# Kernel optimization log

Hardware: AMD Instinct MI355X
Metric: run time of the kernel (lower is better)

Reference implementation:

```python
import jax, jax.numpy as jnp
import numpy as np

# Standard NF4 lookup table (16 quantile values of a normal distribution)
NF4_TABLE = jnp.array([
    -1.0, -0.6961928009986877, -0.5250730514526367, -0.39491748809814453,
    -0.28444138169288635, -0.18477343022823334, -0.09105003625154495, 0.0,
    0.07958029955625534, 0.16093020141124725, 0.24611230194568634,
    0.33791524171829224, 0.44070982933044434, 0.5626170039176941,
    0.7229568362236023, 1.0], dtype=jnp.float32)
BLOCK = 64  # per-block quantization block size


def dequant_nf4(codes, scalers):
    """codes: int [out, in] values in [0,16); scalers: float [out*in/BLOCK]."""
    shape = codes.shape
    vals = NF4_TABLE[codes.reshape(-1, BLOCK)]  # [n_blocks, BLOCK]
    return (vals * scalers[:, None]).reshape(shape)


def setup_inputs() -> dict:
    key = jax.random.key(0)
    ks = jax.random.split(key, 7)
    D, H, T = 4096, 11008, 8192
    nb1 = H * D // BLOCK
    x = jax.random.normal(ks[0], (T, D), dtype=jnp.float32)
    w1_codes = jax.random.randint(ks[1], (H, D), 0, 16, dtype=jnp.int32)
    w1_scalers = jax.random.uniform(ks[2], (nb1,), dtype=jnp.float32) * 0.02
    w2_codes = jax.random.randint(ks[3], (H, D), 0, 16, dtype=jnp.int32)
    w2_scalers = jax.random.uniform(ks[4], (nb1,), dtype=jnp.float32) * 0.02
    w3_codes = jax.random.randint(ks[5], (D, H), 0, 16, dtype=jnp.int32)
    w3_scalers = jax.random.uniform(ks[6], (nb1,), dtype=jnp.float32) * 0.02
    return {"x": x, "w1_codes": w1_codes, "w1_scalers": w1_scalers,
            "w2_codes": w2_codes, "w2_scalers": w2_scalers,
            "w3_codes": w3_codes, "w3_scalers": w3_scalers}


def reference(x, w1_codes, w1_scalers, w2_codes, w2_scalers, w3_codes, w3_scalers):
    w1 = dequant_nf4(w1_codes, w1_scalers)  # [H, D]
    w2 = dequant_nf4(w2_codes, w2_scalers)  # [H, D]
    w3 = dequant_nf4(w3_codes, w3_scalers)  # [D, H]
    h = jax.nn.silu(x @ w1.T) * (x @ w2.T)  # [T, H]
    return h @ w3.T                          # [T, D]
```

## Files before the change

### kernel.cpp

```cpp
#include <hip/hip_runtime.h>
#include <hip/hip_bf16.h>

#define T_DIM 8192
#define D_DIM 4096
#define H_DIM 11008

typedef __attribute__((ext_vector_type(8))) __bf16 bf16x8;
typedef __attribute__((ext_vector_type(4))) float f32x4;

typedef __attribute__((address_space(1))) const void gvoid_t;
typedef __attribute__((address_space(3))) void lvoid_t;

__device__ __forceinline__ void async_lds16(const void* g, void* l) {
    __builtin_amdgcn_global_load_lds((gvoid_t*)g, (lvoid_t*)l, 16, 0, 0);
}

__device__ const float NF4_TAB[16] = {
    -1.0f, -0.6961928009986877f, -0.5250730514526367f, -0.39491748809814453f,
    -0.28444138169288635f, -0.18477343022823334f, -0.09105003625154495f, 0.0f,
    0.07958029955625534f, 0.16093020141124725f, 0.24611230194568634f,
    0.33791524171829224f, 0.44070982933044434f, 0.5626170039176941f,
    0.7229568362236023f, 1.0f};

__global__ void dequant_nf4_kernel(const int* __restrict__ codes,
                                   const float* __restrict__ scalers,
                                   __bf16* __restrict__ out, long n) {
    __shared__ float tbl[16];
    if (threadIdx.x < 16) tbl[threadIdx.x] = NF4_TAB[threadIdx.x];
    __syncthreads();
    long i = ((long)blockIdx.x * blockDim.x + threadIdx.x) * 8;
    if (i >= n) return;
    float s = scalers[i >> 6];
    const int4* cp = (const int4*)(codes + i);
    int4 c0 = cp[0], c1 = cp[1];
    bf16x8 v;
    v[0] = (__bf16)(tbl[c0.x] * s);
    v[1] = (__bf16)(tbl[c0.y] * s);
    v[2] = (__bf16)(tbl[c0.z] * s);
    v[3] = (__bf16)(tbl[c0.w] * s);
    v[4] = (__bf16)(tbl[c1.x] * s);
    v[5] = (__bf16)(tbl[c1.y] * s);
    v[6] = (__bf16)(tbl[c1.z] * s);
    v[7] = (__bf16)(tbl[c1.w] * s);
    *(bf16x8*)(out + i) = v;
}

__global__ void cvt_f32_bf16(const float* __restrict__ x, __bf16* __restrict__ out, long n) {
    long i = ((long)blockIdx.x * blockDim.x + threadIdx.x) * 8;
    if (i >= n) return;
    const float4* xp = (const float4*)(x + i);
    float4 f0 = xp[0], f1 = xp[1];
    bf16x8 v;
    v[0] = (__bf16)f0.x; v[1] = (__bf16)f0.y; v[2] = (__bf16)f0.z; v[3] = (__bf16)f0.w;
    v[4] = (__bf16)f1.x; v[5] = (__bf16)f1.y; v[6] = (__bf16)f1.z; v[7] = (__bf16)f1.w;
    *(bf16x8*)(out + i) = v;
}

template<int KD, int SILU, typename OutT>
__global__ __launch_bounds__(512, 2) void gemm_nt(
    const __bf16* __restrict__ A, const __bf16* __restrict__ B1,
    const __bf16* __restrict__ B2, OutT* __restrict__ Out, const int N)
{
    static_assert(KD % 128 == 0, "need an even number of K-tiles");
    __shared__ __bf16 lds[2 * 2 * 256 * 64];

    const int tid  = threadIdx.x;
    const int lane = tid & 63;
    const int wave = tid >> 6;
    const int wm = wave >> 2;
    const int wn = wave & 3;

    const int nwg  = gridDim.x * gridDim.y;
    const int bid0 = blockIdx.y * gridDim.x + blockIdx.x;
    const int q    = nwg >> 3;
    const int Rr   = q / gridDim.x;
    const int xcd  = bid0 & 7;
    const int j    = bid0 >> 3;
    const int by   = xcd * Rr + (j % Rr);
    const int bx   = j / Rr;
    const long m0 = (long)by * 256;
    const long n0 = (long)bx * (SILU ? 128 : 256);

    const int sr = tid >> 3;
    const int sb = (tid & 7) ^ (sr & 7);
    const __bf16* Arow = A + (m0 + sr) * (long)KD + sb * 8;
    const __bf16* Brow;
    if (SILU) {
        const __bf16* matp = (sr & 16) ? B2 : B1;
        Brow = matp + (n0 + ((sr >> 5) << 4) + (sr & 15)) * (long)KD + sb * 8;
    } else {
        Brow = B1 + (n0 + sr) * (long)KD + sb * 8;
    }
    __bf16* dstA = &lds[(wave << 3) * 64];
    __bf16* dstB = dstA + 16384;

    const long BH = (SILU ? 64 : 128) * (long)KD;
    const long BA = (SILU ? 32 : 64) * (long)KD;

#define STAGE_A(BUF, H, KT) do { \
        const __bf16* s_ = Arow + (long)(H) * 128 * KD + (long)(KT) * 64; \
        __bf16* d_ = dstA + (BUF) * 32768 + (H) * 8192; \
        async_lds16(s_, d_); \
        async_lds16(s_ + 64 * (long)KD, d_ + 4096); \
    } while (0)
#define STAGE_B(BUF, H, KT) do { \
        const __bf16* s_ = Brow + (long)(H) * BH + (long)(KT) * 64; \
        __bf16* d_ = dstB + (BUF) * 32768 + (H) * 8192; \
        async_lds16(s_, d_); \
        async_lds16(s_ + BA, d_ + 4096); \
    } while (0)

    const int r15 = lane & 15;
    const int hi2 = lane >> 4;
    const int l7  = lane & 7;
    const int aOff = (wm * 128 + r15) * 64;
    const int bOff = 16384 + (wn * 64 + r15) * 64;

    auto rdA = [&](int buf, int m, int kk) -> bf16x8 {
        return *(const bf16x8*)&lds[buf * 32768 + aOff + m * 1024 +
                                    (((kk * 4 + hi2) ^ l7) << 3)];
    };
    auto rdB = [&](int buf, int n, int kk) -> bf16x8 {
        return *(const bf16x8*)&lds[buf * 32768 + bOff + n * 1024 +
                                    (((kk * 4 + hi2) ^ l7) << 3)];
    };

    f32x4 acc[8][4];
    const f32x4 z4 = {0.f, 0.f, 0.f, 0.f};
#pragma unroll
    for (int m = 0; m < 8; ++m)
#pragma unroll
        for (int n = 0; n < 4; ++n) acc[m][n] = z4;

    bf16x8 aF[8][2];
    bf16x8 bF[4][2];

#define LOAD_A4(BUF, MB) { _Pragma("unroll") for (int m_ = 0; m_ < 4; ++m_) { \
        aF[m_ + MB][0] = rdA(BUF, m_ + MB, 0); \
        aF[m_ + MB][1] = rdA(BUF, m_ + MB, 1); } }
#define LOAD_B2(BUF, NB) { _Pragma("unroll") for (int n_ = 0; n_ < 2; ++n_) { \
        bF[n_ + NB][0] = rdB(BUF, n_ + NB, 0); \
        bF[n_ + NB][1] = rdB(BUF, n_ + NB, 1); } }
#define QUAD(MB, NB) { _Pragma("unroll") for (int m_ = 0; m_ < 4; ++m_) { \
        _Pragma("unroll") for (int n_ = 0; n_ < 2; ++n_) { \
        acc[m_ + MB][n_ + NB] = __builtin_amdgcn_mfma_f32_16x16x32_bf16( \
            aF[m_ + MB][0], bF[n_ + NB][0], acc[m_ + MB][n_ + NB], 0, 0, 0); \
        acc[m_ + MB][n_ + NB] = __builtin_amdgcn_mfma_f32_16x16x32_bf16( \
            aF[m_ + MB][1], bF[n_ + NB][1], acc[m_ + MB][n_ + NB], 0, 0, 0); } } }
#define BAR()  __builtin_amdgcn_s_barrier()
#define LGK0() asm volatile("s_waitcnt lgkmcnt(0)" ::: "memory")
#define VM6()  asm volatile("s_waitcnt vmcnt(6)" ::: "memory")
#define PRIO1() __builtin_amdgcn_s_setprio(1)
#define PRIO0() __builtin_amdgcn_s_setprio(0)

#define TILE(BUF, T1, T2) \
    LOAD_A4(BUF, 0); LOAD_B2(BUF, 0); \
    STAGE_B(1 - (BUF), 1, T1); \
    BAR(); LGK0(); PRIO1(); QUAD(0, 0); PRIO0(); BAR(); \
    LOAD_A4(BUF, 4); LOAD_B2(BUF, 2); \
    BAR(); LGK0(); PRIO1(); QUAD(0, 2); PRIO0(); BAR(); \
    STAGE_A(BUF, 0, T2); STAGE_A(BUF, 1, T2); \
    PRIO1(); QUAD(4, 2); PRIO0(); \
    STAGE_B(BUF, 0, T2); \
    PRIO1(); QUAD(4, 0); PRIO0(); \
    VM6(); BAR();

    const int NT = KD / 64;

    STAGE_A(0, 0, 0); STAGE_A(0, 1, 0);
    STAGE_B(0, 0, 0); STAGE_B(0, 1, 0);
    STAGE_A(1, 0, 1); STAGE_A(1, 1, 1);
    STAGE_B(1, 0, 1);
    VM6();
    BAR();

#pragma unroll 1
    for (int t = 0; t < NT; t += 2) {
        const int t1 = t + 1;
        int t2 = t + 2; if (t2 >= NT) t2 -= NT;
        int t3 = t + 3; if (t3 >= NT) t3 -= NT;
        TILE(0, t1, t2);
        TILE(1, t2, t3);
    }
    asm volatile("s_waitcnt vmcnt(0)" ::: "memory");

    const int crow = hi2 * 4;
    if (SILU) {
#pragma unroll
        for (int m = 0; m < 8; ++m)
#pragma unroll
            for (int p = 0; p < 2; ++p)
#pragma unroll
                for (int r = 0; r < 4; ++r) {
                    const long row = m0 + wm * 128 + m * 16 + crow + r;
                    const long idx = row * (long)N + (n0 + wn * 32 + p * 16 + r15);
                    float a = acc[m][2 * p][r];
                    float b = acc[m][2 * p + 1][r];
                    float sg = 1.0f / (1.0f + __expf(-a));
                    Out[idx] = (OutT)(a * sg * b);
                }
    } else {
#pragma unroll
        for (int m = 0; m < 8; ++m)
#pragma unroll
            for (int n = 0; n < 4; ++n)
#pragma unroll
                for (int r = 0; r < 4; ++r) {
                    const long row = m0 + wm * 128 + m * 16 + crow + r;
                    const long idx = row * (long)N + (n0 + wn * 64 + n * 16 + r15);
                    Out[idx] = (OutT)acc[m][n][r];
                }
    }
#undef STAGE_A
#undef STAGE_B
#undef LOAD_A4
#undef LOAD_B2
#undef QUAD
#undef TILE
#undef BAR
#undef LGK0
#undef VM6
#undef PRIO1
#undef PRIO0
}

extern "C" void kernel_launch(void* const* d_in, const int* in_sizes, int n_in,
                              void* d_out, int out_size, void* d_ws, size_t ws_size,
                              hipStream_t stream) {
    const float* x   = (const float*)d_in[0];
    const int*   w1c = (const int*)d_in[1];
    const float* w1s = (const float*)d_in[2];
    const int*   w2c = (const int*)d_in[3];
    const float* w2s = (const float*)d_in[4];
    const int*   w3c = (const int*)d_in[5];
    const float* w3s = (const float*)d_in[6];
    float* out = (float*)d_out;

    char* ws = (char*)d_ws;
    __bf16* xb  = (__bf16*)ws;  ws += (size_t)T_DIM * D_DIM * 2;
    __bf16* w1b = (__bf16*)ws;  ws += (size_t)H_DIM * D_DIM * 2;
    __bf16* w2b = (__bf16*)ws;  ws += (size_t)H_DIM * D_DIM * 2;
    __bf16* w3b = (__bf16*)ws;  ws += (size_t)H_DIM * D_DIM * 2;
    __bf16* hb  = (__bf16*)ws;

    const long nx = (long)T_DIM * D_DIM;
    const long nw = (long)H_DIM * D_DIM;

    cvt_f32_bf16<<<(int)(nx / (256 * 8)), 256, 0, stream>>>(x, xb, nx);
    dequant_nf4_kernel<<<(int)(nw / (256 * 8)), 256, 0, stream>>>(w1c, w1s, w1b, nw);
    dequant_nf4_kernel<<<(int)(nw / (256 * 8)), 256, 0, stream>>>(w2c, w2s, w2b, nw);
    dequant_nf4_kernel<<<(int)(nw / (256 * 8)), 256, 0, stream>>>(w3c, w3s, w3b, nw);

    gemm_nt<D_DIM, 1, __bf16><<<dim3(H_DIM / 128, T_DIM / 256), 512, 0, stream>>>(
        xb, w1b, w2b, hb, H_DIM);
    gemm_nt<H_DIM, 0, float><<<dim3(D_DIM / 256, T_DIM / 256), 512, 0, stream>>>(
        hb, w3b, nullptr, out, D_DIM);
}
```

Baseline: 2.300 ms.

## Restructure GEMM main loop to overlap LDS fragment reads with MFMA quadrants

Reorders the double-buffered GEMM inner loop so LDS fragment reads for the next quadrant, and for the next tile's first quadrant, are issued ahead of the current MFMA work. Partial lgkmcnt waits replace full drains, and sched_barrier pins the ordering. Global-to-LDS staging is rescheduled: both B halves are staged together, and vmcnt is drained once per tile instead of keeping 6 loads in flight. The aim is to hide LDS latency and cut full waits, at the cost of more barriers per tile and tighter, hand-counted wait correctness.

```diff
diff --git a/kernel.cpp b/kernel.cpp
--- a/kernel.cpp
+++ b/kernel.cpp
@@ -135,12 +135,14 @@
     bf16x8 aF[8][2];
     bf16x8 bF[4][2];
 
-#define LOAD_A4(BUF, MB) { _Pragma("unroll") for (int m_ = 0; m_ < 4; ++m_) { \
-        aF[m_ + MB][0] = rdA(BUF, m_ + MB, 0); \
-        aF[m_ + MB][1] = rdA(BUF, m_ + MB, 1); } }
-#define LOAD_B2(BUF, NB) { _Pragma("unroll") for (int n_ = 0; n_ < 2; ++n_) { \
-        bF[n_ + NB][0] = rdB(BUF, n_ + NB, 0); \
-        bF[n_ + NB][1] = rdB(BUF, n_ + NB, 1); } }
+#define RD_A03(BUF) { _Pragma("unroll") for (int m_ = 0; m_ < 4; ++m_) { \
+        aF[m_][0] = rdA(BUF, m_, 0); aF[m_][1] = rdA(BUF, m_, 1); } }
+#define RD_A47(BUF) { _Pragma("unroll") for (int m_ = 4; m_ < 8; ++m_) { \
+        aF[m_][0] = rdA(BUF, m_, 0); aF[m_][1] = rdA(BUF, m_, 1); } }
+#define RD_B01(BUF) { _Pragma("unroll") for (int n_ = 0; n_ < 2; ++n_) { \
+        bF[n_][0] = rdB(BUF, n_, 0); bF[n_][1] = rdB(BUF, n_, 1); } }
+#define RD_B23(BUF) { _Pragma("unroll") for (int n_ = 2; n_ < 4; ++n_) { \
+        bF[n_][0] = rdB(BUF, n_, 0); bF[n_][1] = rdB(BUF, n_, 1); } }
 #define QUAD(MB, NB) { _Pragma("unroll") for (int m_ = 0; m_ < 4; ++m_) { \
         _Pragma("unroll") for (int n_ = 0; n_ < 2; ++n_) { \
         acc[m_ + MB][n_ + NB] = __builtin_amdgcn_mfma_f32_16x16x32_bf16( \
@@ -148,41 +150,55 @@
         acc[m_ + MB][n_ + NB] = __builtin_amdgcn_mfma_f32_16x16x32_bf16( \
             aF[m_ + MB][1], bF[n_ + NB][1], acc[m_ + MB][n_ + NB], 0, 0, 0); } } }
 #define BAR()  __builtin_amdgcn_s_barrier()
-#define LGK0() asm volatile("s_waitcnt lgkmcnt(0)" ::: "memory")
-#define VM6()  asm volatile("s_waitcnt vmcnt(6)" ::: "memory")
+#define LGK(n) do { asm volatile("s_waitcnt lgkmcnt(" #n ")" ::: "memory"); \
+                    __builtin_amdgcn_sched_barrier(0); } while (0)
+#define VMC(n) do { asm volatile("s_waitcnt vmcnt(" #n ")" ::: "memory"); \
+                    __builtin_amdgcn_sched_barrier(0); } while (0)
 #define PRIO1() __builtin_amdgcn_s_setprio(1)
 #define PRIO0() __builtin_amdgcn_s_setprio(0)
 
-#define TILE(BUF, T1, T2) \
-    LOAD_A4(BUF, 0); LOAD_B2(BUF, 0); \
-    STAGE_B(1 - (BUF), 1, T1); \
-    BAR(); LGK0(); PRIO1(); QUAD(0, 0); PRIO0(); BAR(); \
-    LOAD_A4(BUF, 4); LOAD_B2(BUF, 2); \
-    BAR(); LGK0(); PRIO1(); QUAD(0, 2); PRIO0(); BAR(); \
+#define TILE(BUF, T2) \
+     \
+    RD_B23(BUF); \
+    LGK(4); \
+    PRIO1(); QUAD(0, 0); PRIO0(); \
+     \
+    BAR(); \
+    RD_A47(BUF); \
+    LGK(8); \
+    PRIO1(); QUAD(0, 2); PRIO0(); \
+    VMC(0); \
+     \
+    BAR(); \
+    STAGE_B(BUF, 0, T2); STAGE_B(BUF, 1, T2); \
+    RD_A03(1 - (BUF)); \
+    LGK(8); \
+    PRIO1(); QUAD(4, 0); PRIO0(); \
+     \
+    BAR(); \
     STAGE_A(BUF, 0, T2); STAGE_A(BUF, 1, T2); \
-    PRIO1(); QUAD(4, 2); PRIO0(); \
-    STAGE_B(BUF, 0, T2); \
-    PRIO1(); QUAD(4, 0); PRIO0(); \
-    VM6(); BAR();
+    RD_B01(1 - (BUF)); \
+    PRIO1(); QUAD(4, 2); PRIO0();
 
     const int NT = KD / 64;
 
     STAGE_A(0, 0, 0); STAGE_A(0, 1, 0);
     STAGE_B(0, 0, 0); STAGE_B(0, 1, 0);
+    STAGE_B(1, 0, 1); STAGE_B(1, 1, 1);
     STAGE_A(1, 0, 1); STAGE_A(1, 1, 1);
-    STAGE_B(1, 0, 1);
-    VM6();
+    VMC(8);
     BAR();
+    RD_A03(0);
+    RD_B01(0);
 
 #pragma unroll 1
     for (int t = 0; t < NT; t += 2) {
-        const int t1 = t + 1;
         int t2 = t + 2; if (t2 >= NT) t2 -= NT;
         int t3 = t + 3; if (t3 >= NT) t3 -= NT;
-        TILE(0, t1, t2);
-        TILE(1, t2, t3);
+        TILE(0, t2);
+        TILE(1, t3);
     }
-    asm volatile("s_waitcnt vmcnt(0)" ::: "memory");
+    asm volatile("s_waitcnt vmcnt(0) lgkmcnt(0)" ::: "memory");
 
     const int crow = hi2 * 4;
     if (SILU) {
@@ -213,13 +229,15 @@
     }
 #undef STAGE_A
 #undef STAGE_B
-#undef LOAD_A4
-#undef LOAD_B2
+#undef RD_A03
+#undef RD_A47
+#undef RD_B01
+#undef RD_B23
 #undef QUAD
 #undef TILE
 #undef BAR
-#undef LGK0
-#undef VM6
+#undef LGK
+#undef VMC
 #undef PRIO1
 #undef PRIO0
 }
```

New measurement: 2.780 ms. 1.21x slower.
